# Optimization experiments

Hardware: AMD Instinct MI355X
Metric: run time of the kernel (lower is better)

Reference implementation:

```python
import jax, jax.numpy as jnp
import numpy as np

B, N, D = 1, 4096, 320
HEADS, DIM_HEAD = 8, 40
PHASE, Hm, Wm = 3, 64, 64  # guidance mask spatial dims; Hm*Wm == N


def setup_inputs() -> dict:
    key = jax.random.key(0)
    ks = jax.random.split(key, 7)
    s = 0.02
    x = jax.random.normal(ks[0], (B, N, D), jnp.float32)
    guidance_mask = jax.random.bernoulli(ks[1], 0.25, (B, PHASE, Hm, Wm)).astype(jnp.float32)
    Wq = jax.random.normal(ks[2], (D, HEADS * DIM_HEAD), jnp.float32) * s
    Wk = jax.random.normal(ks[3], (D, HEADS * DIM_HEAD), jnp.float32) * s
    Wv = jax.random.normal(ks[4], (D, HEADS * DIM_HEAD), jnp.float32) * s
    Wo = jax.random.normal(ks[5], (HEADS * DIM_HEAD, D), jnp.float32) * s
    bo = jnp.zeros((D,), jnp.float32)
    return {"x": x, "guidance_mask": guidance_mask, "Wq": Wq, "Wk": Wk,
            "Wv": Wv, "Wo": Wo, "bo": bo}


def reference(x, guidance_mask, Wq, Wk, Wv, Wo, bo):
    b, n, _ = x.shape
    h, dh = HEADS, DIM_HEAD
    scale = dh ** (-0.5)

    def split_heads(t):
        # b n (h d) -> (b h) n d
        return t.reshape(b, n, h, dh).transpose(0, 2, 1, 3).reshape(b * h, n, dh)

    q = split_heads(x @ Wq)
    k = split_heads(x @ Wk)
    v = split_heads(x @ Wv)

    sim = jnp.einsum('bid,bjd->bij', q, k) * scale  # (b*h, n, n)

    _, p, Hh, Ww = guidance_mask.shape
    HW = Hh * Ww  # == n
    g = guidance_mask.reshape(b, p, HW)
    # sum over phases of outer products, clamped at 1 (binary block mask)
    mask_sim = jnp.minimum(jnp.einsum('bpi,bpj->bij', g, g), 1.0)  # (b, HW, HW)
    mask_sim = jnp.repeat(mask_sim, h, axis=0)  # (b*h, HW, HW), heads within each b

    neg = -jnp.finfo(sim.dtype).max
    # original: sim[:, :, :HW][mask_sim == 0] = -max ; here n == HW so full matrix
    sim = jnp.where(mask_sim == 0, neg, sim)

    attn = jax.nn.softmax(sim, axis=-1)
    out = jnp.einsum('bij,bjd->bid', attn, v)  # (b*h, n, dh)
    out = out.reshape(b, h, n, dh).transpose(0, 2, 1, 3).reshape(b, n, h * dh)
    return out @ Wo + bo
```

## Files before the change

kernel.cpp:

```cpp
#include <hip/hip_runtime.h>
#include <hip/hip_bf16.h>
#include <stdint.h>

#define NT 4096
#define DM 320
#define NH 8
#define DH 40
#define KS 4
#define QSCALE 0.22811013f
#define PSTR 68
#define KFJB 640

typedef float f32x4 __attribute__((ext_vector_type(4)));
typedef __bf16 bf16x8 __attribute__((ext_vector_type(8)));

__device__ __forceinline__ unsigned short f2b(float f) {
  unsigned u = __builtin_bit_cast(unsigned, f);
  u += 0x7FFFu + ((u >> 16) & 1u);
  return (unsigned short)(u >> 16);
}

__device__ __forceinline__ bf16x8 ld_bf8(const unsigned short* p) {
  uint4 v = *(const uint4*)p;
  return __builtin_bit_cast(bf16x8, v);
}

__device__ __forceinline__ f32x4 mfma16(bf16x8 a, bf16x8 b, f32x4 c) {
  return __builtin_amdgcn_mfma_f32_16x16x32_bf16(a, b, c, 0, 0, 0);
}

__device__ __forceinline__ float fexp2(float x) {
#if __has_builtin(__builtin_amdgcn_exp2f)
  return __builtin_amdgcn_exp2f(x);
#else
  float r; asm("v_exp_f32 %0, %1" : "=v"(r) : "v"(x)); return r;
#endif
}

__device__ __forceinline__ uint2 pack4(float a, float b, float c, float d) {
  uint2 pk;
  pk.x = (unsigned)f2b(a) | ((unsigned)f2b(b) << 16);
  pk.y = (unsigned)f2b(c) | ((unsigned)f2b(d) << 16);
  return pk;
}

__device__ __forceinline__ size_t fmi(int tile, int nk, int k, int o) {
  return ((size_t)tile * nk + (k >> 5)) * 512 + (size_t)((k >> 3) & 3) * 128 +
         (size_t)(o & 15) * 8 + (k & 7);
}

__global__ __launch_bounds__(256) void prep_kernel(
    const float* __restrict__ x, const float* __restrict__ g,
    const float* __restrict__ Wq, const float* __restrict__ Wk,
    const float* __restrict__ Wv, const float* __restrict__ Wo,
    unsigned short* __restrict__ xbf, unsigned char* __restrict__ sigb,
    unsigned short* __restrict__ Wtf, int* __restrict__ perm,
    int* __restrict__ nqp) {
  const int b = blockIdx.x, t = threadIdx.x;
  if (b == 100) {
    __shared__ int cnt[256];
    unsigned char mys[16];
    int c1 = 0;
#pragma unroll
    for (int i = 0; i < 16; ++i) {
      int tok = t * 16 + i;
      unsigned s = 0;
      if (g[tok] != 0.f)          s |= 1u;
      if (g[NT + tok] != 0.f)     s |= 2u;
      if (g[2 * NT + tok] != 0.f) s |= 4u;
      sigb[tok] = (unsigned char)s;
      mys[i] = (unsigned char)s;
      c1 += (s != 0u);
    }
    cnt[t] = c1;
    __syncthreads();
    for (int off = 1; off < 256; off <<= 1) {
      int v = (t >= off) ? cnt[t - off] : 0;
      __syncthreads();
      cnt[t] += v;
      __syncthreads();
    }
    const int nq = cnt[255];
    int p1 = cnt[t] - c1;
    int p0 = nq + (t * 16 - p1);
#pragma unroll
    for (int i = 0; i < 16; ++i) {
      int tok = t * 16 + i;
      if (mys[i] != 0) perm[p1++] = tok;
      else             perm[p0++] = tok;
    }
    if (t == 0) nqp[0] = nq;
    return;
  }
  if (b > 100) {
    int base = (b - 101) * 2560;
#pragma unroll
    for (int j = 0; j < 10; ++j) {
      int i = (base + j * 256 + t) * 4;
      int m = i / DM, k = i % DM;
      float4 v = *(const float4*)(x + i);
      ushort4 u;
      u.x = f2b(v.x); u.y = f2b(v.y); u.z = f2b(v.z); u.w = f2b(v.w);
      *(ushort4*)(xbf + fmi(m >> 4, 10, k, m)) = u;
    }
    return;
  }
  __shared__ __align__(16) unsigned short lt[64 * 72];
  int kx = b % 5, cy = b / 5;
  int cm = cy % 5;
  const float* src;
  int rowbase;
  if (cy < 5)       { src = Wq; rowbase = cm * 64; }
  else if (cy < 10) { src = Wk; rowbase = 320 + cm * 64; }
  else if (cy < 15) { src = Wv; rowbase = 640 + cm * 64; }
  else              { src = Wo; rowbase = 960 + cm * 64; }
  const int c0 = cm * 64;
  const int k0 = kx * 64;
#pragma unroll
  for (int i = 0; i < 4; ++i) {
    int kr = (t >> 4) + i * 16, cc = (t & 15) * 4;
    float4 w4 = *(const float4*)&src[(size_t)(k0 + kr) * DM + c0 + cc];
    lt[(cc + 0) * 72 + kr] = f2b(w4.x);
    lt[(cc + 1) * 72 + kr] = f2b(w4.y);
    lt[(cc + 2) * 72 + kr] = f2b(w4.z);
    lt[(cc + 3) * 72 + kr] = f2b(w4.w);
  }
  __syncthreads();
#pragma unroll
  for (int i = 0; i < 2; ++i) {
    int idx = t + i * 256, cl = idx >> 3, ch = idx & 7;
    int c = rowbase + cl, k = k0 + ch * 8;
    *(uint4*)&Wtf[fmi(c >> 4, 10, k, c)] = *(const uint4*)&lt[cl * 72 + ch * 8];
  }
}

__global__ __launch_bounds__(256, 4) void qkv_gemm(
    const unsigned short* __restrict__ xbf, const unsigned short* __restrict__ Wtf,
    unsigned short* __restrict__ Qb, unsigned short* __restrict__ Kf,
    unsigned short* __restrict__ Vf) {
  const int t = threadIdx.x;
  const int w = t >> 6, lane = t & 63, quad = lane >> 4, ln = lane & 15;
  const int m0 = blockIdx.x * 64;
  const int cy = blockIdx.y;
  const int a = cy / 5;
  const int cc0 = (cy % 5) * 64;
  const int mt = (m0 >> 4) + w;
  const int ct0 = a * 20 + (cc0 >> 4);

  f32x4 acc[4] = {{0,0,0,0},{0,0,0,0},{0,0,0,0},{0,0,0,0}};
  for (int kc = 0; kc < 10; ++kc) {
    bf16x8 xf = ld_bf8(xbf + ((size_t)(mt * 10 + kc)) * 512 + lane * 8);
#pragma unroll
    for (int nt = 0; nt < 4; ++nt) {
      bf16x8 wf = ld_bf8(Wtf + ((size_t)((ct0 + nt) * 10 + kc)) * 512 + lane * 8);
      if (a < 2) acc[nt] = mfma16(wf, xf, acc[nt]);
      else       acc[nt] = mfma16(xf, wf, acc[nt]);
    }
  }
  if (a == 0) {
    const int m = m0 + w * 16 + ln;
#pragma unroll
    for (int nt = 0; nt < 4; ++nt) {
      int c = cc0 + nt * 16 + quad * 4;
      int h = c / DH, d = c % DH;
      uint2 pk = pack4(acc[nt][0] * QSCALE, acc[nt][1] * QSCALE,
                       acc[nt][2] * QSCALE, acc[nt][3] * QSCALE);
      *(uint2*)&Qb[((size_t)h * NT + m) * 64 + d] = pk;
    }
  } else if (a == 1) {
    const int m = m0 + w * 16 + ln;
#pragma unroll
    for (int nt = 0; nt < 4; ++nt) {
      int c = cc0 + nt * 16 + quad * 4;
      int h = c / DH, d = c % DH;
      uint2 pk = pack4(acc[nt][0], acc[nt][1], acc[nt][2], acc[nt][3]);
      size_t base = ((size_t)h * 256 + (m >> 4)) * KFJB;
      size_t idx = (d < 32)
          ? base + (size_t)(d >> 3) * 128 + (size_t)(m & 15) * 8 + (d & 7)
          : base + 512 + (size_t)(m & 15) * 8 + (d - 32);
      *(uint2*)&Kf[idx] = pk;
    }
  } else {
    const int mb = m0 + w * 16 + quad * 4;
#pragma unroll
    for (int nt = 0; nt < 4; ++nt) {
      int c = cc0 + nt * 16 + ln;
      int h = c / DH, d = c % DH;
      uint2 pk = pack4(acc[nt][0], acc[nt][1], acc[nt][2], acc[nt][3]);
      size_t idx = ((((((size_t)(h * 64 + (mb >> 6)) * 3 + (d >> 4)) * 2 +
                       ((mb >> 5) & 1)) * 4 + ((mb >> 3) & 3)) * 16 + (d & 15))) * 8 +
                   (mb & 7);
      *(uint2*)&Vf[idx] = pk;
    }
  }
}

__global__ __launch_bounds__(256, 4) void attn_kernel(
    const unsigned short* __restrict__ Qb, const unsigned short* __restrict__ Kf,
    const unsigned short* __restrict__ Vf, const unsigned char* __restrict__ sigb,
    const int* __restrict__ perm, const int* __restrict__ nqp,
    unsigned short* __restrict__ Opf, float* __restrict__ Lpart) {
  __shared__ __align__(16) unsigned short pt[4][32 * PSTR];
  const int t = threadIdx.x;
  const int w = t >> 6, lane = t & 63, quad = lane >> 4, ln = lane & 15;
  const int h = blockIdx.y, sp = blockIdx.z;
  const int qt = (blockIdx.x + 8 * sp) & 31;
  const int qrow = qt * 128 + w * 32;
  const int j0 = sp * 16;
  const int nq_pad = (nqp[0] + 127) & ~127;
  const bool writer = (qt * 128 >= nq_pad);

  const unsigned short* Kfh = Kf + (size_t)h * 256 * KFJB;
  const unsigned short* Vfh = Vf + (size_t)h * 196608;
  unsigned short* ptw = pt[w];
  const uint4 z4 = {0, 0, 0, 0};
  const uint4 ones4 = {0x3F803F80u, 0x3F803F80u, 0x3F803F80u, 0x3F803F80u};
  const bf16x8 onesb = __builtin_bit_cast(bf16x8, ones4);
  const bool vone = (ln == 8);

  bf16x8 qa[2][2];
  unsigned sqx4[2], uqx4[2];
  int morig[2];
  f32x4 o[3][2] = {{{0,0,0,0},{0,0,0,0}},{{0,0,0,0},{0,0,0,0}},{{0,0,0,0},{0,0,0,0}}};

#pragma unroll
  for (int tq = 0; tq < 2; ++tq) {
    int bp = qrow + tq * 16 + ln;
    int mo = perm[bp];
    morig[tq] = mo;
    if (!writer) {
      const unsigned short* Qp = Qb + ((size_t)h * NT + mo) * 64;
      qa[tq][0] = ld_bf8(Qp + quad * 8);
      uint4 q1 = z4;
      if (quad == 0) q1 = *(const uint4*)(Qp + 32);
      qa[tq][1] = __builtin_bit_cast(bf16x8, q1);
      unsigned s = sigb[mo];
      sqx4[tq] = s * 0x01010101u;
      uqx4[tq] = (s == 0u) ? 0xFFFFFFFFu : 0u;
      if (s == 0u) {
        qa[tq][0] = __builtin_bit_cast(bf16x8, z4);
        qa[tq][1] = __builtin_bit_cast(bf16x8, z4);
      }
    }
  }

  for (int jt = j0; jt < j0 + 16; ++jt) {
    if (!writer) {
      uint4 kfr0[4], kfr1[4];
#pragma unroll
      for (int nt = 0; nt < 4; ++nt) {
        const unsigned short* kb = Kfh + (size_t)(jt * 4 + nt) * KFJB;
        kfr0[nt] = *(const uint4*)(kb + lane * 8);
        kfr1[nt] = z4;
        if (lane < 16) kfr1[nt] = *(const uint4*)(kb + 512 + lane * 8);
      }
#pragma unroll
      for (int nt = 0; nt < 4; ++nt) {
        bf16x8 ka0 = __builtin_bit_cast(bf16x8, kfr0[nt]);
        bf16x8 ka1 = __builtin_bit_cast(bf16x8, kfr1[nt]);
        unsigned spj = *(const unsigned*)(sigb + jt * 64 + nt * 16 + quad * 4);
#pragma unroll
        for (int tq = 0; tq < 2; ++tq) {
          f32x4 acc = {0.f, 0.f, 0.f, 0.f};
          acc = mfma16(ka0, qa[tq][0], acc);
          acc = mfma16(ka1, qa[tq][1], acc);
          unsigned m4 = (spj & sqx4[tq]) | uqx4[tq];
          unsigned u[4];
#pragma unroll
          for (int r = 0; r < 4; ++r) {
            unsigned mb = (m4 >> (8 * r)) & 255u;
            float am = mb ? acc[r] : -3.0e38f;
            u[r] = __builtin_bit_cast(unsigned, fexp2(am));
          }
          uint2 pk;
          pk.x = (u[0] >> 16) | (u[1] & 0xffff0000u);
          pk.y = (u[2] >> 16) | (u[3] & 0xffff0000u);
          *(uint2*)&ptw[(tq * 16 + ln) * PSTR + nt * 16 + quad * 4] = pk;
        }
      }
    }
    uint4 vfr[6];
#pragma unroll
    for (int ot = 0; ot < 3; ++ot)
#pragma unroll
      for (int c = 0; c < 2; ++c)
        vfr[ot * 2 + c] =
            *(const uint4*)(Vfh + ((size_t)((jt * 3 + ot) * 2 + c)) * 512 + lane * 8);
    if (vone) { vfr[4] = ones4; vfr[5] = ones4; }

    bf16x8 pb[2][2];
    if (!writer) {
      asm volatile("s_waitcnt lgkmcnt(0)" ::: "memory");
#pragma unroll
      for (int tq = 0; tq < 2; ++tq) {
        pb[tq][0] = ld_bf8(&ptw[(tq * 16 + ln) * PSTR + quad * 8]);
        pb[tq][1] = ld_bf8(&ptw[(tq * 16 + ln) * PSTR + 32 + quad * 8]);
      }
    } else {
      pb[0][0] = onesb; pb[0][1] = onesb; pb[1][0] = onesb; pb[1][1] = onesb;
    }
#pragma unroll
    for (int ot = 0; ot < 3; ++ot) {
      bf16x8 va0 = __builtin_bit_cast(bf16x8, vfr[ot * 2]);
      bf16x8 va1 = __builtin_bit_cast(bf16x8, vfr[ot * 2 + 1]);
#pragma unroll
      for (int tq = 0; tq < 2; ++tq) {
        o[ot][tq] = mfma16(va0, pb[tq][0], o[ot][tq]);
        o[ot][tq] = mfma16(va1, pb[tq][1], o[ot][tq]);
      }
    }
  }

#pragma unroll
  for (int tq = 0; tq < 2; ++tq) {
    int m = morig[tq];
#pragma unroll
    for (int ot = 0; ot < 3; ++ot) {
      int d0 = ot * 16 + quad * 4;
      if (d0 < DH) {
        int c = h * DH + d0;
        uint2 pk = pack4(o[ot][tq][0], o[ot][tq][1], o[ot][tq][2], o[ot][tq][3]);
        *(uint2*)&Opf[fmi(sp * 256 + (m >> 4), 10, c, m)] = pk;
      }
    }
    if (quad == 2)
      Lpart[sp * NT + m] = o[2][tq][0];
  }
}

__global__ __launch_bounds__(256, 4) void out_gemm(
    const unsigned short* __restrict__ Opf, const float* __restrict__ Lpart,
    const unsigned short* __restrict__ Wtf, const float* __restrict__ bo,
    float* __restrict__ out) {
  const int t = threadIdx.x;
  const int w = t >> 6, lane = t & 63, quad = lane >> 4, ln = lane & 15;
  const int m0 = blockIdx.x * 64;
  const int cc0 = blockIdx.y * 64;
  const int mt = (m0 >> 4) + w;
  const int m = m0 + w * 16 + ln;
  const int ct0 = 60 + (cc0 >> 4);
  float ls = 0.f;
#pragma unroll
  for (int sp = 0; sp < KS; ++sp) ls += Lpart[sp * NT + m];
  const float inv = 1.f / ls;

  f32x4 acc[4] = {{0,0,0,0},{0,0,0,0},{0,0,0,0},{0,0,0,0}};
  for (int kc = 0; kc < 10; ++kc) {
    float s8[8] = {0, 0, 0, 0, 0, 0, 0, 0};
#pragma unroll
    for (int sp = 0; sp < KS; ++sp) {
      uint4 v = *(const uint4*)(Opf + ((size_t)((sp * 256 + mt) * 10 + kc)) * 512 +
                                lane * 8);
      unsigned vv[4] = {v.x, v.y, v.z, v.w};
#pragma unroll
      for (int j = 0; j < 4; ++j) {
        s8[2 * j]     += __builtin_bit_cast(float, vv[j] << 16);
        s8[2 * j + 1] += __builtin_bit_cast(float, vv[j] & 0xffff0000u);
      }
    }
    unsigned short af8[8];
#pragma unroll
    for (int j = 0; j < 8; ++j) af8[j] = f2b(s8[j] * inv);
    bf16x8 af = ld_bf8(af8);
#pragma unroll
    for (int nt = 0; nt < 4; ++nt) {
      bf16x8 wf = ld_bf8(Wtf + ((size_t)((ct0 + nt) * 10 + kc)) * 512 + lane * 8);
      acc[nt] = mfma16(wf, af, acc[nt]);
    }
  }
#pragma unroll
  for (int nt = 0; nt < 4; ++nt) {
    int c = cc0 + nt * 16 + quad * 4;
    float4 bv = *(const float4*)(bo + c);
    float4 ov;
    ov.x = acc[nt][0] + bv.x;
    ov.y = acc[nt][1] + bv.y;
    ov.z = acc[nt][2] + bv.z;
    ov.w = acc[nt][3] + bv.w;
    *(float4*)(out + (size_t)m * DM + c) = ov;
  }
}

extern "C" void kernel_launch(void* const* d_in, const int* in_sizes, int n_in,
                              void* d_out, int out_size, void* d_ws, size_t ws_size,
                              hipStream_t stream) {
  const float* x  = (const float*)d_in[0];
  const float* g  = (const float*)d_in[1];
  const float* Wq = (const float*)d_in[2];
  const float* Wk = (const float*)d_in[3];
  const float* Wv = (const float*)d_in[4];
  const float* Wo = (const float*)d_in[5];
  const float* bo = (const float*)d_in[6];
  float* out = (float*)d_out;

  char* ws = (char*)d_ws;
  const size_t SIG_OFF  = 0;
  const size_t NQ_OFF   = 4096;
  const size_t PERM_OFF = 8192;
  const size_t XBF_OFF  = 32768;
  const size_t WTF_OFF = XBF_OFF + (size_t)NT * DM * 2;
  const size_t QB_OFF  = WTF_OFF + (size_t)1280 * DM * 2;
  const size_t KF_OFF  = QB_OFF + (size_t)NH * NT * 64 * 2;
  const size_t VF_OFF  = KF_OFF + (size_t)NH * 256 * KFJB * 2;
  const size_t OPF_OFF = VF_OFF + (size_t)NH * 196608 * 2;
  const size_t LP_OFF  = OPF_OFF + (size_t)KS * 256 * 10 * 512 * 2;
  unsigned char* sigb  = (unsigned char*)(ws + SIG_OFF);
  int* nqp             = (int*)(ws + NQ_OFF);
  int* perm            = (int*)(ws + PERM_OFF);
  unsigned short* xbf  = (unsigned short*)(ws + XBF_OFF);
  unsigned short* Wtf  = (unsigned short*)(ws + WTF_OFF);
  unsigned short* Qb   = (unsigned short*)(ws + QB_OFF);
  unsigned short* Kf   = (unsigned short*)(ws + KF_OFF);
  unsigned short* Vf   = (unsigned short*)(ws + VF_OFF);
  unsigned short* Opf  = (unsigned short*)(ws + OPF_OFF);
  float* Lpart         = (float*)(ws + LP_OFF);

  prep_kernel<<<229, 256, 0, stream>>>(x, g, Wq, Wk, Wv, Wo, xbf, sigb, Wtf,
                                       perm, nqp);
  qkv_gemm<<<dim3(64, 15), 256, 0, stream>>>(xbf, Wtf, Qb, Kf, Vf);
  attn_kernel<<<dim3(32, NH, KS), 256, 0, stream>>>(Qb, Kf, Vf, sigb, perm, nqp,
                                                    Opf, Lpart);
  out_gemm<<<dim3(64, 5), 256, 0, stream>>>(Opf, Lpart, Wtf, bo, out);
}
```

Before: 140.4 us.

## Store Q/K/V in permuted order and skip masked-out key tiles in attention

The prep kernel now builds an inverse permutation and a permuted signature array, and the QKV GEMM writes Q, K and V directly into permuted token order. With all masked tokens grouped first, attention query tiles that are fully active only loop over key tiles up to the active count, skipping key tiles made only of zero-signature tokens. The key-split is also changed from contiguous to strided tiles for balance. In exchange, V stores become scalar scattered 2-byte writes instead of packed 8-byte writes, which may slow the GEMM epilogue.

```diff
diff --git a/kernel.cpp b/kernel.cpp
--- a/kernel.cpp
+++ b/kernel.cpp
@@ -53,9 +53,9 @@
     const float* __restrict__ x, const float* __restrict__ g,
     const float* __restrict__ Wq, const float* __restrict__ Wk,
     const float* __restrict__ Wv, const float* __restrict__ Wo,
-    unsigned short* __restrict__ xbf, unsigned char* __restrict__ sigb,
+    unsigned short* __restrict__ xbf, unsigned char* __restrict__ sgp,
     unsigned short* __restrict__ Wtf, int* __restrict__ perm,
-    int* __restrict__ nqp) {
+    int* __restrict__ invp, int* __restrict__ nqp) {
   const int b = blockIdx.x, t = threadIdx.x;
   if (b == 100) {
     __shared__ int cnt[256];
@@ -68,7 +68,6 @@
       if (g[tok] != 0.f)          s |= 1u;
       if (g[NT + tok] != 0.f)     s |= 2u;
       if (g[2 * NT + tok] != 0.f) s |= 4u;
-      sigb[tok] = (unsigned char)s;
       mys[i] = (unsigned char)s;
       c1 += (s != 0u);
     }
@@ -86,8 +85,8 @@
 #pragma unroll
     for (int i = 0; i < 16; ++i) {
       int tok = t * 16 + i;
-      if (mys[i] != 0) perm[p1++] = tok;
-      else             perm[p0++] = tok;
+      if (mys[i] != 0) { perm[p1] = tok; invp[tok] = p1; sgp[p1] = mys[i]; p1++; }
+      else             { perm[p0] = tok; invp[tok] = p0; sgp[p0] = 0;      p0++; }
     }
     if (t == 0) nqp[0] = nq;
     return;
@@ -136,6 +135,7 @@
 
 __global__ __launch_bounds__(256, 4) void qkv_gemm(
     const unsigned short* __restrict__ xbf, const unsigned short* __restrict__ Wtf,
+    const int* __restrict__ invp,
     unsigned short* __restrict__ Qb, unsigned short* __restrict__ Kf,
     unsigned short* __restrict__ Vf) {
   const int t = threadIdx.x;
@@ -158,46 +158,52 @@
     }
   }
   if (a == 0) {
-    const int m = m0 + w * 16 + ln;
+    const int bp = invp[m0 + w * 16 + ln];
 #pragma unroll
     for (int nt = 0; nt < 4; ++nt) {
       int c = cc0 + nt * 16 + quad * 4;
       int h = c / DH, d = c % DH;
       uint2 pk = pack4(acc[nt][0] * QSCALE, acc[nt][1] * QSCALE,
                        acc[nt][2] * QSCALE, acc[nt][3] * QSCALE);
-      *(uint2*)&Qb[((size_t)h * NT + m) * 64 + d] = pk;
+      *(uint2*)&Qb[((size_t)h * NT + bp) * 64 + d] = pk;
     }
   } else if (a == 1) {
-    const int m = m0 + w * 16 + ln;
+    const int bp = invp[m0 + w * 16 + ln];
 #pragma unroll
     for (int nt = 0; nt < 4; ++nt) {
       int c = cc0 + nt * 16 + quad * 4;
       int h = c / DH, d = c % DH;
       uint2 pk = pack4(acc[nt][0], acc[nt][1], acc[nt][2], acc[nt][3]);
-      size_t base = ((size_t)h * 256 + (m >> 4)) * KFJB;
+      size_t base = ((size_t)h * 256 + (bp >> 4)) * KFJB;
       size_t idx = (d < 32)
-          ? base + (size_t)(d >> 3) * 128 + (size_t)(m & 15) * 8 + (d & 7)
-          : base + 512 + (size_t)(m & 15) * 8 + (d - 32);
+          ? base + (size_t)(d >> 3) * 128 + (size_t)(bp & 15) * 8 + (d & 7)
+          : base + 512 + (size_t)(bp & 15) * 8 + (d - 32);
       *(uint2*)&Kf[idx] = pk;
     }
   } else {
     const int mb = m0 + w * 16 + quad * 4;
+    int bpr[4];
+#pragma unroll
+    for (int r = 0; r < 4; ++r) bpr[r] = invp[mb + r];
 #pragma unroll
     for (int nt = 0; nt < 4; ++nt) {
       int c = cc0 + nt * 16 + ln;
       int h = c / DH, d = c % DH;
-      uint2 pk = pack4(acc[nt][0], acc[nt][1], acc[nt][2], acc[nt][3]);
-      size_t idx = ((((((size_t)(h * 64 + (mb >> 6)) * 3 + (d >> 4)) * 2 +
-                       ((mb >> 5) & 1)) * 4 + ((mb >> 3) & 3)) * 16 + (d & 15))) * 8 +
-                   (mb & 7);
-      *(uint2*)&Vf[idx] = pk;
+#pragma unroll
+      for (int r = 0; r < 4; ++r) {
+        int bp = bpr[r];
+        size_t idx = ((((((size_t)(h * 64 + (bp >> 6)) * 3 + (d >> 4)) * 2 +
+                         ((bp >> 5) & 1)) * 4 + ((bp >> 3) & 3)) * 16 + (d & 15))) * 8 +
+                     (bp & 7);
+        Vf[idx] = f2b(acc[nt][r]);
+      }
     }
   }
 }
 
 __global__ __launch_bounds__(256, 4) void attn_kernel(
     const unsigned short* __restrict__ Qb, const unsigned short* __restrict__ Kf,
-    const unsigned short* __restrict__ Vf, const unsigned char* __restrict__ sigb,
+    const unsigned short* __restrict__ Vf, const unsigned char* __restrict__ sgp,
     const int* __restrict__ perm, const int* __restrict__ nqp,
     unsigned short* __restrict__ Opf, float* __restrict__ Lpart) {
   __shared__ __align__(16) unsigned short pt[4][32 * PSTR];
@@ -206,9 +212,11 @@
   const int h = blockIdx.y, sp = blockIdx.z;
   const int qt = (blockIdx.x + 8 * sp) & 31;
   const int qrow = qt * 128 + w * 32;
-  const int j0 = sp * 16;
-  const int nq_pad = (nqp[0] + 127) & ~127;
+  const int nq = nqp[0];
+  const int nkt = (nq + 63) >> 6;
+  const int nq_pad = (nq + 127) & ~127;
   const bool writer = (qt * 128 >= nq_pad);
+  const int jt_end = (!writer && (qt + 1) * 128 <= nq) ? nkt : 64;
 
   const unsigned short* Kfh = Kf + (size_t)h * 256 * KFJB;
   const unsigned short* Vfh = Vf + (size_t)h * 196608;
@@ -226,15 +234,14 @@
 #pragma unroll
   for (int tq = 0; tq < 2; ++tq) {
     int bp = qrow + tq * 16 + ln;
-    int mo = perm[bp];
-    morig[tq] = mo;
+    morig[tq] = perm[bp];
     if (!writer) {
-      const unsigned short* Qp = Qb + ((size_t)h * NT + mo) * 64;
+      const unsigned short* Qp = Qb + ((size_t)h * NT + bp) * 64;
       qa[tq][0] = ld_bf8(Qp + quad * 8);
       uint4 q1 = z4;
       if (quad == 0) q1 = *(const uint4*)(Qp + 32);
       qa[tq][1] = __builtin_bit_cast(bf16x8, q1);
-      unsigned s = sigb[mo];
+      unsigned s = sgp[bp];
       sqx4[tq] = s * 0x01010101u;
       uqx4[tq] = (s == 0u) ? 0xFFFFFFFFu : 0u;
       if (s == 0u) {
@@ -244,7 +251,7 @@
     }
   }
 
-  for (int jt = j0; jt < j0 + 16; ++jt) {
+  for (int jt = sp; jt < jt_end; jt += KS) {
     if (!writer) {
       uint4 kfr0[4], kfr1[4];
 #pragma unroll
@@ -258,7 +265,7 @@
       for (int nt = 0; nt < 4; ++nt) {
         bf16x8 ka0 = __builtin_bit_cast(bf16x8, kfr0[nt]);
         bf16x8 ka1 = __builtin_bit_cast(bf16x8, kfr1[nt]);
-        unsigned spj = *(const unsigned*)(sigb + jt * 64 + nt * 16 + quad * 4);
+        unsigned spj = *(const unsigned*)(sgp + jt * 64 + nt * 16 + quad * 4);
 #pragma unroll
         for (int tq = 0; tq < 2; ++tq) {
           f32x4 acc = {0.f, 0.f, 0.f, 0.f};
@@ -394,19 +401,21 @@
   float* out = (float*)d_out;
 
   char* ws = (char*)d_ws;
-  const size_t SIG_OFF  = 0;
+  const size_t SGP_OFF  = 0;
   const size_t NQ_OFF   = 4096;
   const size_t PERM_OFF = 8192;
-  const size_t XBF_OFF  = 32768;
+  const size_t INV_OFF  = 24576;
+  const size_t XBF_OFF  = 40960;
   const size_t WTF_OFF = XBF_OFF + (size_t)NT * DM * 2;
   const size_t QB_OFF  = WTF_OFF + (size_t)1280 * DM * 2;
   const size_t KF_OFF  = QB_OFF + (size_t)NH * NT * 64 * 2;
   const size_t VF_OFF  = KF_OFF + (size_t)NH * 256 * KFJB * 2;
   const size_t OPF_OFF = VF_OFF + (size_t)NH * 196608 * 2;
   const size_t LP_OFF  = OPF_OFF + (size_t)KS * 256 * 10 * 512 * 2;
-  unsigned char* sigb  = (unsigned char*)(ws + SIG_OFF);
+  unsigned char* sgp   = (unsigned char*)(ws + SGP_OFF);
   int* nqp             = (int*)(ws + NQ_OFF);
   int* perm            = (int*)(ws + PERM_OFF);
+  int* invp            = (int*)(ws + INV_OFF);
   unsigned short* xbf  = (unsigned short*)(ws + XBF_OFF);
   unsigned short* Wtf  = (unsigned short*)(ws + WTF_OFF);
   unsigned short* Qb   = (unsigned short*)(ws + QB_OFF);
@@ -415,10 +424,10 @@
   unsigned short* Opf  = (unsigned short*)(ws + OPF_OFF);
   float* Lpart         = (float*)(ws + LP_OFF);
 
-  prep_kernel<<<229, 256, 0, stream>>>(x, g, Wq, Wk, Wv, Wo, xbf, sigb, Wtf,
-                                       perm, nqp);
-  qkv_gemm<<<dim3(64, 15), 256, 0, stream>>>(xbf, Wtf, Qb, Kf, Vf);
-  attn_kernel<<<dim3(32, NH, KS), 256, 0, stream>>>(Qb, Kf, Vf, sigb, perm, nqp,
+  prep_kernel<<<229, 256, 0, stream>>>(x, g, Wq, Wk, Wv, Wo, xbf, sgp, Wtf,
+                                       perm, invp, nqp);
+  qkv_gemm<<<dim3(64, 15), 256, 0, stream>>>(xbf, Wtf, invp, Qb, Kf, Vf);
+  attn_kernel<<<dim3(32, NH, KS), 256, 0, stream>>>(Qb, Kf, Vf, sgp, perm, nqp,
                                                     Opf, Lpart);
   out_gemm<<<dim3(64, 5), 256, 0, stream>>>(Opf, Lpart, Wtf, bo, out);
 }
```

Measured after the change: 138.4 us (median of 2 runs). Within noise of the previous version (-1.4%).
